# Kernel optimization log

Hardware: AMD Instinct MI355X
Metric: run time of the kernel (lower is better)

## Reference

```python
import jax, jax.numpy as jnp
import numpy as np
import math

D_K = 8  # = n_wires; one input value encoded per wire


def setup_inputs() -> dict:
    key = jax.random.key(0)
    k1, k2, k3, k4 = jax.random.split(key, 4)
    B, S, E = 4, 2048, 1024
    x = jax.random.normal(k1, (B, S, E), dtype=jnp.float32)
    theta = jax.random.normal(k2, (D_K,), dtype=jnp.float32)  # shared RX params (one ModuleList reused per head)
    W = jax.random.normal(k3, (E, E), dtype=jnp.float32) * (1.0 / math.sqrt(E))
    b = jax.random.normal(k4, (E,), dtype=jnp.float32) * 0.01
    return {"x": x, "theta": theta, "W": W, "b": b}


def reference(x, theta, W, b):
    B, S, E = x.shape
    dk = theta.shape[0]
    H = E // dk
    # Quantum circuit collapse: RX(x_i) then RX(theta_i) on |0>, measure PauliZ
    # on each wire of a product state -> <Z_i> = cos(x_i + theta_i).
    proj = x.reshape(B, S, H, dk)
    q_out = jnp.cos(proj + theta)  # theta broadcast over (B,S,H)
    # NOTE: faithful to original — attention is over the HEAD axis: (B,S,H,H)
    attn = jnp.einsum('bshd,bsgd->bshg', q_out, q_out) / math.sqrt(dk)
    attn = jax.nn.softmax(attn, axis=-1)  # dropout is identity at inference
    out = jnp.einsum('bshg,bsgd->bshd', attn, q_out)  # (B,S,H,dk)
    # faithful transpose(1,2).contiguous().view(B,S,E) reinterleave
    out = jnp.transpose(out, (0, 2, 1, 3)).reshape(B, S, E)
    return out @ W.T + b
```

## Files before the change

kernel.cpp:

```cpp
#include <hip/hip_runtime.h>
#include <hip/hip_bf16.h>
#include <stdint.h>

typedef __attribute__((ext_vector_type(8))) short bf16x8;
typedef __attribute__((ext_vector_type(4))) float f32x4;
typedef __attribute__((ext_vector_type(16))) float f32x16;
typedef __attribute__((ext_vector_type(2))) unsigned int uint32x2;
typedef __attribute__((address_space(3))) void lds_t;
typedef __attribute__((address_space(1))) void glb_t;

#define B_ 4
#define S_ 2048
#define E_ 1024
#define M_ (B_*S_)

static __device__ __forceinline__ ushort f2bf(float f) {
  uint32_t u = __float_as_uint(f);
  u += 0x7fffu + ((u >> 16) & 1u);
  return (ushort)(u >> 16);
}

static __device__ __forceinline__ uint32_t pk_bf16(float lo, float hi) {
  uint32_t r;
  asm("v_cvt_pk_bf16_f32 %0, %1, %2" : "=v"(r) : "v"(lo), "v"(hi));
  return r;
}
static __device__ __forceinline__ float fexp2(float x) {
  float r;
  asm("v_exp_f32 %0, %1" : "=v"(r) : "v"(x));
  return r;
}

static __device__ __forceinline__ void half_zip(uint32_t a, uint32_t b, bool convA,
                                                uint32_t& X, uint32_t& Y) {
  if (convA) {
    uint32x2 r = __builtin_amdgcn_permlane32_swap(b, a, false, false);
    Y = r[0]; X = r[1];
  } else {
    uint32x2 r = __builtin_amdgcn_permlane32_swap(a, b, false, false);
    X = r[0]; Y = r[1];
  }
}

__global__ __launch_bounds__(256) void qattn(const float* __restrict__ x,
                                             const float* __restrict__ theta,
                                             ushort* __restrict__ outr) {
  const int wave = threadIdx.x >> 6;
  const int lane = threadIdx.x & 63;
  const int bid = blockIdx.x;
  const int bs = (bid & 7) * 1024 + (bid >> 3);
  const int b = bs >> 11, s = bs & 2047;
  const int l31 = lane & 31, hw = lane >> 5;

  __shared__ __align__(16) ushort qp[129 * 8];
  __shared__ __align__(16) ushort qt[16 * 144];

  uint32x2 pr = __builtin_amdgcn_permlane32_swap((uint32_t)lane, (uint32_t)(lane + 1000),
                                                 false, false);
  const bool convA = (__builtin_amdgcn_readfirstlane((int)pr[0]) >= 1000);

  {
    const int h  = 32 * wave + (lane >> 1);
    const int dh = (lane & 1) * 4;
    const float4 xv = *(const float4*)(x + (size_t)bs * E_ + h * 8 + dh);
    float q[4];
    q[0] = __cosf(xv.x + theta[dh + 0]);
    q[1] = __cosf(xv.y + theta[dh + 1]);
    q[2] = __cosf(xv.z + theta[dh + 2]);
    q[3] = __cosf(xv.w + theta[dh + 3]);

    const float QS = 0.71419165f;
    uint2 pw;
    pw.x = pk_bf16(q[0] * QS, q[1] * QS);
    pw.y = pk_bf16(q[2] * QS, q[3] * QS);
    *(uint2*)(qp + h * 8 + dh) = pw;

    #pragma unroll
    for (int j = 0; j < 4; ++j)
      qt[(dh + j) * 144 + h] = f2bf(q[j]);
    #pragma unroll
    for (int j = 0; j < 4; ++j)
      qt[(8 + dh + j) * 144 + h] = (j == 0) ? (ushort)0x3F80u : (ushort)0u;

    if (lane == 0) *(uint4*)(qp + 128 * 8) = make_uint4(0, 0, 0, 0);
  }
  __syncthreads();
  __builtin_amdgcn_sched_barrier(0);

  bf16x8 qtf[8];
  const bf16x8 zf = {};
  #pragma unroll
  for (int ks = 0; ks < 8; ++ks) {
    bf16x8 f = *(const bf16x8*)(qt + (l31 & 15) * 144 + ks * 16 + hw * 8);
    qtf[ks] = (l31 < 16) ? f : zf;
  }

  const int hi = wave;
  const int brow = (lane < 32) ? (hi * 32 + l31) : 128;
  const bf16x8 bq = *(const bf16x8*)(qp + brow * 8);

  f32x16 oacc = {};

  #pragma unroll
  for (int gj = 0; gj < 4; ++gj) {
    const int arow = (lane < 32) ? (gj * 32 + l31) : 128;
    const bf16x8 aq = *(const bf16x8*)(qp + arow * 8);
    f32x16 sc = {};
    sc = __builtin_amdgcn_mfma_f32_32x32x16_bf16(aq, bq, sc, 0, 0, 0);
    float p[16];
    #pragma unroll
    for (int i = 0; i < 16; ++i) p[i] = fexp2(sc[i]);
    #pragma unroll
    for (int sl = 0; sl < 2; ++sl) {
      const int pb = sl * 8;
      const uint32_t u = pk_bf16(p[pb+0], p[pb+1]);
      const uint32_t v = pk_bf16(p[pb+2], p[pb+3]);
      const uint32_t w = pk_bf16(p[pb+4], p[pb+5]);
      const uint32_t z = pk_bf16(p[pb+6], p[pb+7]);
      uint32_t f0, f1, f2, f3;
      half_zip(u, w, convA, f0, f2);
      half_zip(v, z, convA, f1, f3);
      uint32_t fr[4] = {f0, f1, f2, f3};
      oacc = __builtin_amdgcn_mfma_f32_32x32x16_bf16(qtf[gj*2 + sl], *(const bf16x8*)fr,
                                                     oacc, 0, 0, 0);
    }
  }

  const int scol = s & 127, srow = s >> 7;
  const float inv = __builtin_amdgcn_rcpf(oacc[4]);
  const uint32_t o01 = pk_bf16(oacc[0] * inv, oacc[1] * inv);
  const uint32_t o23 = pk_bf16(oacc[2] * inv, oacc[3] * inv);
  const int h = hi * 32 + l31;
  const size_t row = (size_t)(b * 2048 + h * 16 + srow);
  *(uint2*)(outr + row * E_ + scol * 8 + hw * 4) = make_uint2(o01, o23);
}

__global__ __launch_bounds__(256) void wconv(const float* __restrict__ W,
                                             ushort* __restrict__ Wb) {
  const int i = blockIdx.x * 256 + threadIdx.x;
  const float4 v = ((const float4*)W)[i];
  ushort4 o;
  o.x = f2bf(v.x); o.y = f2bf(v.y); o.z = f2bf(v.z); o.w = f2bf(v.w);
  ((ushort4*)Wb)[i] = o;
}

__global__ __launch_bounds__(256) void gemm_bt(const ushort* __restrict__ A,
                                               const ushort* __restrict__ Bw,
                                               const float* __restrict__ bias,
                                               float* __restrict__ C) {
  __shared__ __align__(16) ushort As[128 * 32];
  __shared__ __align__(16) ushort Bs[128 * 32];

  const int t = threadIdx.x;
  const int lane = t & 63;
  const int wavei = t >> 6;
  const int wr = wavei >> 1, wc = wavei & 1;
  const int lhi = lane >> 4, llo = lane & 15;
  const size_t ar0 = (size_t)blockIdx.x * 128;
  const size_t br0 = (size_t)blockIdx.y * 128;

  const int c0 = t, c1 = t + 256;
  const int r0 = c0 >> 2, kp0 = (c0 & 3) * 8;
  const int r1 = c1 >> 2, kp1 = (c1 & 3) * 8;

  f32x4 acc[4][4] = {};

  for (int k0 = 0; k0 < E_; k0 += 32) {
    __builtin_amdgcn_global_load_lds((const glb_t*)(A  + (ar0 + r0) * E_ + k0 + kp0),
                                     (lds_t*)(As + c0 * 8), 16, 0, 0);
    __builtin_amdgcn_global_load_lds((const glb_t*)(A  + (ar0 + r1) * E_ + k0 + kp1),
                                     (lds_t*)(As + c1 * 8), 16, 0, 0);
    __builtin_amdgcn_global_load_lds((const glb_t*)(Bw + (br0 + r0) * E_ + k0 + kp0),
                                     (lds_t*)(Bs + c0 * 8), 16, 0, 0);
    __builtin_amdgcn_global_load_lds((const glb_t*)(Bw + (br0 + r1) * E_ + k0 + kp1),
                                     (lds_t*)(Bs + c1 * 8), 16, 0, 0);
    __syncthreads();

    bf16x8 af[4], bfr[4];
    #pragma unroll
    for (int i = 0; i < 4; ++i)
      af[i] = *(const bf16x8*)(As + (wr * 64 + i * 16 + llo) * 32 + lhi * 8);
    #pragma unroll
    for (int j = 0; j < 4; ++j)
      bfr[j] = *(const bf16x8*)(Bs + (wc * 64 + j * 16 + llo) * 32 + lhi * 8);

    #pragma unroll
    for (int i = 0; i < 4; ++i)
      #pragma unroll
      for (int j = 0; j < 4; ++j)
        acc[i][j] = __builtin_amdgcn_mfma_f32_16x16x32_bf16(af[i], bfr[j], acc[i][j], 0, 0, 0);

    __syncthreads();
  }

  #pragma unroll
  for (int j = 0; j < 4; ++j) {
    const int n = (int)br0 + wc * 64 + j * 16 + llo;
    const float bj = bias[n];
    #pragma unroll
    for (int i = 0; i < 4; ++i) {
      const int mb = (int)ar0 + wr * 64 + i * 16 + lhi * 4;
      #pragma unroll
      for (int r = 0; r < 4; ++r) {
        C[(size_t)(mb + r) * E_ + n] = acc[i][j][r] + bj;
      }
    }
  }
}

extern "C" void kernel_launch(void* const* d_in, const int* in_sizes, int n_in,
                              void* d_out, int out_size, void* d_ws, size_t ws_size,
                              hipStream_t stream) {
  const float* x     = (const float*)d_in[0];
  const float* theta = (const float*)d_in[1];
  const float* W     = (const float*)d_in[2];
  const float* bias  = (const float*)d_in[3];
  float* out = (float*)d_out;

  ushort* outr = (ushort*)d_ws;
  ushort* Wb   = (ushort*)((char*)d_ws + (size_t)M_ * E_ * 2);

  qattn<<<M_, 256, 0, stream>>>(x, theta, outr);
  wconv<<<(E_ * E_) / (256 * 4), 256, 0, stream>>>(W, Wb);
  dim3 g(M_ / 128, E_ / 128);
  gemm_bt<<<g, 256, 0, stream>>>(outr, Wb, bias, out);
}
```

Baseline: 69.27 us.

## Process four positions per qattn block with double-buffered LDS prefetch

Each qattn block now handles four consecutive (b,s) positions instead of one. It double-buffers the cos-projected Q tiles in shared memory so the next position's global load and cos generation overlap the current position's MFMA and softmax work. This amortizes block launch and setup overhead, such as the permlane probe, and changes the transposed-tile row stride. It costs an extra barrier per position and fewer total blocks, which may reduce latency hiding.

```diff
diff --git a/kernel.cpp b/kernel.cpp
--- a/kernel.cpp
+++ b/kernel.cpp
@@ -13,6 +13,8 @@
 #define S_ 2048
 #define E_ 1024
 #define M_ (B_*S_)
+#define QTS 152
+#define NPOS 4
 
 static __device__ __forceinline__ ushort f2bf(float f) {
   uint32_t u = __float_as_uint(f);
@@ -47,22 +49,24 @@
                                              ushort* __restrict__ outr) {
   const int wave = threadIdx.x >> 6;
   const int lane = threadIdx.x & 63;
+  const int l31 = lane & 31, hw = lane >> 5;
+
   const int bid = blockIdx.x;
-  const int bs = (bid & 7) * 1024 + (bid >> 3);
-  const int b = bs >> 11, s = bs & 2047;
-  const int l31 = lane & 31, hw = lane >> 5;
-
-  __shared__ __align__(16) ushort qp[129 * 8];
-  __shared__ __align__(16) ushort qt[16 * 144];
+  const int base = ((bid & 7) * 256 + (bid >> 3)) * NPOS;
+
+  __shared__ __align__(16) ushort qL[2][129 * 8];
+  __shared__ __align__(16) ushort qT[2][16 * QTS];
 
   uint32x2 pr = __builtin_amdgcn_permlane32_swap((uint32_t)lane, (uint32_t)(lane + 1000),
                                                  false, false);
   const bool convA = (__builtin_amdgcn_readfirstlane((int)pr[0]) >= 1000);
 
-  {
+  auto gen = [&](int bs_g, int sel) {
+    ushort* qpg = qL[sel];
+    ushort* qtg = qT[sel];
     const int h  = 32 * wave + (lane >> 1);
     const int dh = (lane & 1) * 4;
-    const float4 xv = *(const float4*)(x + (size_t)bs * E_ + h * 8 + dh);
+    const float4 xv = *(const float4*)(x + (size_t)bs_g * E_ + h * 8 + dh);
     float q[4];
     q[0] = __cosf(xv.x + theta[dh + 0]);
     q[1] = __cosf(xv.y + theta[dh + 1]);
@@ -73,66 +77,82 @@
     uint2 pw;
     pw.x = pk_bf16(q[0] * QS, q[1] * QS);
     pw.y = pk_bf16(q[2] * QS, q[3] * QS);
-    *(uint2*)(qp + h * 8 + dh) = pw;
+    *(uint2*)(qpg + h * 8 + dh) = pw;
 
     #pragma unroll
     for (int j = 0; j < 4; ++j)
-      qt[(dh + j) * 144 + h] = f2bf(q[j]);
+      qtg[(dh + j) * QTS + h] = f2bf(q[j]);
     #pragma unroll
     for (int j = 0; j < 4; ++j)
-      qt[(8 + dh + j) * 144 + h] = (j == 0) ? (ushort)0x3F80u : (ushort)0u;
-
-    if (lane == 0) *(uint4*)(qp + 128 * 8) = make_uint4(0, 0, 0, 0);
-  }
+      qtg[(8 + dh + j) * QTS + h] = (j == 0) ? (ushort)0x3F80u : (ushort)0u;
+
+    if (lane == 0) *(uint4*)(qpg + 128 * 8) = make_uint4(0, 0, 0, 0);
+  };
+
+  gen(base, 0);
   __syncthreads();
   __builtin_amdgcn_sched_barrier(0);
 
-  bf16x8 qtf[8];
-  const bf16x8 zf = {};
   #pragma unroll
-  for (int ks = 0; ks < 8; ++ks) {
-    bf16x8 f = *(const bf16x8*)(qt + (l31 & 15) * 144 + ks * 16 + hw * 8);
-    qtf[ks] = (l31 < 16) ? f : zf;
-  }
-
-  const int hi = wave;
-  const int brow = (lane < 32) ? (hi * 32 + l31) : 128;
-  const bf16x8 bq = *(const bf16x8*)(qp + brow * 8);
-
-  f32x16 oacc = {};
-
-  #pragma unroll
-  for (int gj = 0; gj < 4; ++gj) {
-    const int arow = (lane < 32) ? (gj * 32 + l31) : 128;
-    const bf16x8 aq = *(const bf16x8*)(qp + arow * 8);
-    f32x16 sc = {};
-    sc = __builtin_amdgcn_mfma_f32_32x32x16_bf16(aq, bq, sc, 0, 0, 0);
-    float p[16];
-    #pragma unroll
-    for (int i = 0; i < 16; ++i) p[i] = fexp2(sc[i]);
-    #pragma unroll
-    for (int sl = 0; sl < 2; ++sl) {
-      const int pb = sl * 8;
-      const uint32_t u = pk_bf16(p[pb+0], p[pb+1]);
-      const uint32_t v = pk_bf16(p[pb+2], p[pb+3]);
-      const uint32_t w = pk_bf16(p[pb+4], p[pb+5]);
-      const uint32_t z = pk_bf16(p[pb+6], p[pb+7]);
-      uint32_t f0, f1, f2, f3;
-      half_zip(u, w, convA, f0, f2);
-      half_zip(v, z, convA, f1, f3);
-      uint32_t fr[4] = {f0, f1, f2, f3};
-      oacc = __builtin_amdgcn_mfma_f32_32x32x16_bf16(qtf[gj*2 + sl], *(const bf16x8*)fr,
-                                                     oacc, 0, 0, 0);
+  for (int i = 0; i < NPOS; ++i) {
+    const int sel = i & 1;
+    if (i + 1 < NPOS) gen(base + i + 1, sel ^ 1);
+
+    const ushort* qp = qL[sel];
+    const ushort* qt = qT[sel];
+    const int bs = base + i;
+    const int b = bs >> 11, s = bs & 2047;
+
+    bf16x8 qtf[8];
+    const bf16x8 zf = {};
+    #pragma unroll
+    for (int ks = 0; ks < 8; ++ks) {
+      bf16x8 f = *(const bf16x8*)(qt + (l31 & 15) * QTS + ks * 16 + hw * 8);
+      qtf[ks] = (l31 < 16) ? f : zf;
     }
-  }
-
-  const int scol = s & 127, srow = s >> 7;
-  const float inv = __builtin_amdgcn_rcpf(oacc[4]);
-  const uint32_t o01 = pk_bf16(oacc[0] * inv, oacc[1] * inv);
-  const uint32_t o23 = pk_bf16(oacc[2] * inv, oacc[3] * inv);
-  const int h = hi * 32 + l31;
-  const size_t row = (size_t)(b * 2048 + h * 16 + srow);
-  *(uint2*)(outr + row * E_ + scol * 8 + hw * 4) = make_uint2(o01, o23);
+
+    const int hi = wave;
+    const int brow = (lane < 32) ? (hi * 32 + l31) : 128;
+    const bf16x8 bq = *(const bf16x8*)(qp + brow * 8);
+
+    f32x16 oacc = {};
+
+    #pragma unroll
+    for (int gj = 0; gj < 4; ++gj) {
+      const int arow = (lane < 32) ? (gj * 32 + l31) : 128;
+      const bf16x8 aq = *(const bf16x8*)(qp + arow * 8);
+      f32x16 sc = {};
+      sc = __builtin_amdgcn_mfma_f32_32x32x16_bf16(aq, bq, sc, 0, 0, 0);
+      float pv[16];
+      #pragma unroll
+      for (int k = 0; k < 16; ++k) pv[k] = fexp2(sc[k]);
+      #pragma unroll
+      for (int sl = 0; sl < 2; ++sl) {
+        const int pb = sl * 8;
+        const uint32_t u = pk_bf16(pv[pb+0], pv[pb+1]);
+        const uint32_t v = pk_bf16(pv[pb+2], pv[pb+3]);
+        const uint32_t w = pk_bf16(pv[pb+4], pv[pb+5]);
+        const uint32_t z = pk_bf16(pv[pb+6], pv[pb+7]);
+        uint32_t f0, f1, f2, f3;
+        half_zip(u, w, convA, f0, f2);
+        half_zip(v, z, convA, f1, f3);
+        uint32_t fr[4] = {f0, f1, f2, f3};
+        oacc = __builtin_amdgcn_mfma_f32_32x32x16_bf16(qtf[gj*2 + sl], *(const bf16x8*)fr,
+                                                       oacc, 0, 0, 0);
+      }
+    }
+
+    const int scol = s & 127, srow = s >> 7;
+    const float inv = __builtin_amdgcn_rcpf(oacc[4]);
+    const uint32_t o01 = pk_bf16(oacc[0] * inv, oacc[1] * inv);
+    const uint32_t o23 = pk_bf16(oacc[2] * inv, oacc[3] * inv);
+    const int h = hi * 32 + l31;
+    const size_t row = (size_t)(b * 2048 + h * 16 + srow);
+    *(uint2*)(outr + row * E_ + scol * 8 + hw * 4) = make_uint2(o01, o23);
+
+    __syncthreads();
+    __builtin_amdgcn_sched_barrier(0);
+  }
 }
 
 __global__ __launch_bounds__(256) void wconv(const float* __restrict__ W,
@@ -220,7 +240,7 @@
   ushort* outr = (ushort*)d_ws;
   ushort* Wb   = (ushort*)((char*)d_ws + (size_t)M_ * E_ * 2);
 
-  qattn<<<M_, 256, 0, stream>>>(x, theta, outr);
+  qattn<<<M_ / NPOS, 256, 0, stream>>>(x, theta, outr);
   wconv<<<(E_ * E_) / (256 * 4), 256, 0, stream>>>(W, Wb);
   dim3 g(M_ / 128, E_ / 128);
   gemm_bt<<<g, 256, 0, stream>>>(outr, Wb, bias, out);
```

After: 75.25 us. 1.09x slower.
